# Kernel optimization log

Measured on AMD Instinct MI355X. Metric: run time of the kernel, lower is better.

Reference implementation:

```python
import jax, jax.numpy as jnp
import numpy as np

B = 256
N = 1024
K = 64
BASIS = 8
SINKHORN_ITERS = 1
TEMP = 0.2
EPS = 1e-5


def log_sinkhorn(log_alpha, n_iters=SINKHORN_ITERS, temperature=TEMP):
    la = log_alpha / temperature
    for _ in range(n_iters):
        la = la - jax.scipy.special.logsumexp(la, axis=-1, keepdims=True)
        la = la - jax.scipy.special.logsumexp(la, axis=-2, keepdims=True)
    return jnp.exp(la)


def setup_inputs() -> dict:
    key = jax.random.key(0)
    k1, k2, k3, k4 = jax.random.split(key, 4)
    x = jax.random.normal(k1, (B, N * K), dtype=jnp.float32)
    A_logits = 0.01 * jax.random.normal(k2, (N, N), dtype=jnp.float32)
    W_1 = 0.01 * jax.random.normal(k3, (N, BASIS), dtype=jnp.float32)
    W_V = 0.01 * jax.random.normal(k4, (BASIS, K, K), dtype=jnp.float32)
    gamma2 = jnp.ones((N,), dtype=jnp.float32)  # LayerNorm(N) weight
    beta2 = jnp.zeros((N,), dtype=jnp.float32)  # LayerNorm(N) bias
    return {"x": x, "A_logits": A_logits, "W_1": W_1, "W_V": W_V,
            "gamma2": gamma2, "beta2": beta2}


def layernorm(x, gamma, beta):
    mu = jnp.mean(x, axis=-1, keepdims=True)
    var = jnp.mean(jnp.square(x - mu), axis=-1, keepdims=True)
    return (x - mu) * jax.lax.rsqrt(var + EPS) * gamma + beta


def reference(x, A_logits, W_1, W_V, gamma2, beta2):
    x_reshaped = x.reshape(B, N, K)
    A = log_sinkhorn(A_logits)                       # [N, N] doubly-stochastic
    W_logits = jnp.einsum('tk,kde->tde', W_1, W_V)   # [N, K, K]
    W = log_sinkhorn(W_logits)                       # per-block doubly-stochastic
    x_local = jnp.einsum('bni,nio->bno', x_reshaped, W)  # N independent KxK GEMMs
    x_local = layernorm(jnp.transpose(x_local, (0, 2, 1)), gamma2, beta2)  # [B,K,N]
    x_global = x_local @ A                           # [B,K,N]
    x_global = jnp.transpose(x_global, (0, 2, 1))    # [B,N,K]
    return x_global.reshape(B, N * K)
```

## Files before the change

### kernel.cpp

```cpp
#include <hip/hip_runtime.h>
#include <hip/hip_fp16.h>
#include <math.h>

#define NDIM 1024
#define KDIM 64
#define BDIM 256
#define BKDIM 16384

typedef unsigned short u16;
typedef __attribute__((ext_vector_type(8))) short bf16x8;
typedef __attribute__((ext_vector_type(4))) float f32x4;

__device__ __forceinline__ float bf2f(u16 u) {
  union { unsigned u; float f; } x; x.u = ((unsigned)u) << 16; return x.f;
}
__device__ __forceinline__ u16 f2bf(float f) {
  union { float f; unsigned u; } x; x.f = f;
  unsigned u = x.u;
  u += 0x7fffu + ((u >> 16) & 1u);
  return (u16)(u >> 16);
}
__device__ __forceinline__ u16 f2h(float f) { return __half_as_ushort(__float2half(f)); }
__device__ __forceinline__ float h2f(u16 u) { return __half2float(__ushort_as_half(u)); }

__device__ __forceinline__ void async16(const u16* g, u16* s) {
  __builtin_amdgcn_global_load_lds(
      (const __attribute__((address_space(1))) unsigned int*)g,
      (__attribute__((address_space(3))) unsigned int*)s,
      16, 0, 0);
}

__global__ __launch_bounds__(256) void k_row_lse(const float* __restrict__ Alog,
                                                 float* __restrict__ r) {
  int m = blockIdx.x, t = threadIdx.x;
  float v[4], mx = -3.0e38f;
#pragma unroll
  for (int j = 0; j < 4; j++) {
    v[j] = Alog[m * NDIM + t + j * 256] * 5.0f;
    mx = fmaxf(mx, v[j]);
  }
  __shared__ float sred[256];
  sred[t] = mx; __syncthreads();
  for (int s = 128; s > 0; s >>= 1) { if (t < s) sred[t] = fmaxf(sred[t], sred[t + s]); __syncthreads(); }
  float bm = sred[0]; __syncthreads();
  float sm = 0.f;
#pragma unroll
  for (int j = 0; j < 4; j++) sm += __expf(v[j] - bm);
  sred[t] = sm; __syncthreads();
  for (int s = 128; s > 0; s >>= 1) { if (t < s) sred[t] += sred[t + s]; __syncthreads(); }
  if (t == 0) r[m] = bm + __logf(sred[0]);
}

__global__ __launch_bounds__(256) void k_col_dt(const float* __restrict__ Alog,
                                                const float* __restrict__ r,
                                                u16* __restrict__ Dt) {
  int n = blockIdx.x, t = threadIdx.x;
  float v[4], mx = -3.0e38f;
#pragma unroll
  for (int j = 0; j < 4; j++) {
    int m = t + j * 256;
    v[j] = Alog[m * NDIM + n] * 5.0f - r[m];
    mx = fmaxf(mx, v[j]);
  }
  __shared__ float sred[256];
  sred[t] = mx; __syncthreads();
  for (int s = 128; s > 0; s >>= 1) { if (t < s) sred[t] = fmaxf(sred[t], sred[t + s]); __syncthreads(); }
  float bm = sred[0]; __syncthreads();
  float sm = 0.f;
#pragma unroll
  for (int j = 0; j < 4; j++) sm += __expf(v[j] - bm);
  sred[t] = sm; __syncthreads();
  for (int s = 128; s > 0; s >>= 1) { if (t < s) sred[t] += sred[t + s]; __syncthreads(); }
  float cn = bm + __logf(sred[0]);
#pragma unroll
  for (int j = 0; j < 4; j++) {
    int m = t + j * 256;
    Dt[n * NDIM + m] = f2bf(__expf(v[j] - cn) - 0.0009765625f);
  }
}

__global__ __launch_bounds__(256) void k_w(const float* __restrict__ W1,
                                           const float* __restrict__ WV,
                                           u16* __restrict__ Wt) {
  int tb = blockIdx.x, t = threadIdx.x;
  int d = t >> 2, q = t & 3;
  float w1[8];
#pragma unroll
  for (int k = 0; k < 8; k++) w1[k] = W1[tb * 8 + k];
  float la[16];
#pragma unroll
  for (int j = 0; j < 16; j++) la[j] = 0.f;
#pragma unroll
  for (int k = 0; k < 8; k++) {
    float wk = w1[k];
    const float4* base = (const float4*)&WV[k * 4096 + d * 64 + q * 16];
#pragma unroll
    for (int v = 0; v < 4; v++) {
      float4 f = base[v];
      la[v * 4 + 0] += wk * f.x; la[v * 4 + 1] += wk * f.y;
      la[v * 4 + 2] += wk * f.z; la[v * 4 + 3] += wk * f.w;
    }
  }
  float mx = -3.0e38f;
#pragma unroll
  for (int j = 0; j < 16; j++) { la[j] *= 5.0f; mx = fmaxf(mx, la[j]); }
  float sm = 0.f;
#pragma unroll
  for (int j = 0; j < 16; j++) sm += __expf(la[j] - mx);
  for (int off = 1; off < 4; off <<= 1) {
    float mo = __shfl_xor(mx, off), so = __shfl_xor(sm, off);
    float mn = fmaxf(mx, mo);
    sm = sm * __expf(mx - mn) + so * __expf(mo - mn);
    mx = mn;
  }
  float rl = mx + __logf(sm);
  __shared__ float sla[64 * 65];
#pragma unroll
  for (int j = 0; j < 16; j++) sla[d * 65 + q * 16 + j] = la[j] - rl;
  __syncthreads();
  int e = t >> 2, jj = t & 3;
  float lb[16]; float m2 = -3.0e38f;
#pragma unroll
  for (int i = 0; i < 16; i++) { lb[i] = sla[(jj * 16 + i) * 65 + e]; m2 = fmaxf(m2, lb[i]); }
  float s2 = 0.f;
#pragma unroll
  for (int i = 0; i < 16; i++) s2 += __expf(lb[i] - m2);
  for (int off = 1; off < 4; off <<= 1) {
    float mo = __shfl_xor(m2, off), so = __shfl_xor(s2, off);
    float mn = fmaxf(m2, mo);
    s2 = s2 * __expf(m2 - mn) + so * __expf(mo - mn);
    m2 = mn;
  }
  float cl = m2 + __logf(s2);
#pragma unroll
  for (int i = 0; i < 16; i++)
    Wt[tb * 4096 + e * 64 + jj * 16 + i] = f2bf(__expf(lb[i] - cl));
}

__global__ __launch_bounds__(256) void k_gemm1(const float* __restrict__ x,
                                               const u16* __restrict__ Wt,
                                               u16* __restrict__ xl) {
  int n = blockIdx.x, t = threadIdx.x, w = t >> 6, l = t & 63;
  int q = l >> 4, lr = l & 15;
  const float* xb = x + n * 64;
  const u16* wb = Wt + n * 4096;
  f32x4 acc[4][4] = {};
#pragma unroll
  for (int ks = 0; ks < 2; ks++) {
    bf16x8 bfr[4];
#pragma unroll
    for (int ni = 0; ni < 4; ni++)
      bfr[ni] = *(const bf16x8*)&wb[(ni * 16 + lr) * 64 + ks * 32 + q * 8];
#pragma unroll
    for (int mi = 0; mi < 4; mi++) {
      int b = w * 64 + mi * 16 + lr;
      const float* xr = xb + (size_t)b * 65536 + ks * 32 + q * 8;
      float4 v0 = *(const float4*)xr;
      float4 v1 = *(const float4*)(xr + 4);
      float vf[8] = {v0.x, v0.y, v0.z, v0.w, v1.x, v1.y, v1.z, v1.w};
      bf16x8 ah, al;
#pragma unroll
      for (int j = 0; j < 8; j++) {
        u16 h = f2bf(vf[j]);
        ah[j] = (short)h;
        al[j] = (short)f2bf(vf[j] - bf2f(h));
      }
#pragma unroll
      for (int ni = 0; ni < 4; ni++) {
        acc[mi][ni] = __builtin_amdgcn_mfma_f32_16x16x32_bf16(ah, bfr[ni], acc[mi][ni], 0, 0, 0);
        acc[mi][ni] = __builtin_amdgcn_mfma_f32_16x16x32_bf16(al, bfr[ni], acc[mi][ni], 0, 0, 0);
      }
    }
  }
#pragma unroll
  for (int mi = 0; mi < 4; mi++)
#pragma unroll
    for (int ni = 0; ni < 4; ni++) {
      int o = ni * 16 + lr;
#pragma unroll
      for (int reg = 0; reg < 4; reg++) {
        int b = w * 64 + mi * 16 + q * 4 + reg;
        xl[n * BKDIM + b * 64 + o] = f2h(acc[mi][ni][reg]);
      }
    }
}

__global__ __launch_bounds__(256) void k_stat(const u16* __restrict__ xl,
                                              const float* __restrict__ g2,
                                              float* __restrict__ Ps,
                                              float* __restrict__ Pq,
                                              float* __restrict__ Pw) {
  __shared__ float sS[16 * 132], sQ[16 * 132], sW[16 * 132];
  int cb = blockIdx.x, mc = blockIdx.y, t = threadIdx.x;
  int c0 = cb * 128;
  int rg = t >> 4, cs = (t & 15) * 8;
  float sum[8], ssq[8], wg[8];
#pragma unroll
  for (int j = 0; j < 8; j++) { sum[j] = 0.f; ssq[j] = 0.f; wg[j] = 0.f; }
  for (int it = 0; it < 8; it++) {
    int row = mc * 128 + it * 16 + rg;
    bf16x8 v = *(const bf16x8*)&xl[(size_t)row * BKDIM + c0 + cs];
    float gm = g2[row];
#pragma unroll
    for (int j = 0; j < 8; j++) {
      float f = h2f((u16)v[j]);
      sum[j] += f; ssq[j] += f * f; wg[j] += f * gm;
    }
  }
#pragma unroll
  for (int j = 0; j < 8; j++) {
    sS[rg * 132 + cs + j] = sum[j];
    sQ[rg * 132 + cs + j] = ssq[j];
    sW[rg * 132 + cs + j] = wg[j];
  }
  __syncthreads();
  if (t < 128) {
    float S = 0.f, Q = 0.f, W = 0.f;
    for (int k = 0; k < 16; k++) {
      S += sS[k * 132 + t]; Q += sQ[k * 132 + t]; W += sW[k * 132 + t];
    }
    Ps[mc * BKDIM + c0 + t] = S;
    Pq[mc * BKDIM + c0 + t] = Q;
    Pw[mc * BKDIM + c0 + t] = W;
  }
}

__global__ __launch_bounds__(256) void k_fin(const float* __restrict__ Ps,
                                             const float* __restrict__ Pq,
                                             const float* __restrict__ Pw,
                                             const float* __restrict__ g2,
                                             const float* __restrict__ b2,
                                             float* __restrict__ mu,
                                             float* __restrict__ al,
                                             float* __restrict__ sON) {
  __shared__ float red[512];
  int t = threadIdx.x;
  float g = 0.f, b = 0.f;
#pragma unroll
  for (int k = 0; k < 4; k++) { g += g2[t * 4 + k]; b += b2[t * 4 + k]; }
  red[t] = g; red[256 + t] = b; __syncthreads();
  for (int s = 128; s > 0; s >>= 1) {
    if (t < s) { red[t] += red[t + s]; red[256 + t] += red[256 + t + s]; }
    __syncthreads();
  }
  float G = red[0], Bt = red[256];
  int bk = blockIdx.x * 256 + t;
  float S = 0.f, Q = 0.f, W = 0.f;
#pragma unroll
  for (int mc = 0; mc < 8; mc++) {
    S += Ps[mc * BKDIM + bk]; Q += Pq[mc * BKDIM + bk]; W += Pw[mc * BKDIM + bk];
  }
  float m_ = S * (1.0f / 1024.0f);
  float var = Q * (1.0f / 1024.0f) - m_ * m_;
  float a = rsqrtf(var + 1e-5f);
  mu[bk] = m_; al[bk] = a;
  sON[bk] = (a * (W - m_ * G) + Bt) * (1.0f / 1024.0f);
}

__global__ __launch_bounds__(256) void k_apply(const u16* __restrict__ xl,
                                               const float* __restrict__ g2,
                                               const float* __restrict__ b2,
                                               const float* __restrict__ mu,
                                               const float* __restrict__ al,
                                               u16* __restrict__ xln) {
  __shared__ __align__(16) u16 ldsT[128 * 128];
  int bkt = blockIdx.x, mc = blockIdx.y, t = threadIdx.x;
  int c0 = bkt * 128;
  int r = t >> 4, cs = t & 15;
  float mu8[8], al8[8];
#pragma unroll
  for (int j = 0; j < 8; j++) { mu8[j] = mu[c0 + cs * 8 + j]; al8[j] = al[c0 + cs * 8 + j]; }
  int key = cs << 3;
  for (int it = 0; it < 8; it++) {
    int m_ = it * 16 + r;
    int row = mc * 128 + m_;
    bf16x8 v = *(const bf16x8*)&xl[(size_t)row * BKDIM + c0 + cs * 8];
    float gm = g2[row], bt = b2[row];
    int pm = m_ ^ key;
#pragma unroll
    for (int j = 0; j < 8; j++) {
      float f = (h2f((u16)v[j]) - mu8[j]) * al8[j] * gm + bt;
      ldsT[(cs * 8 + j) * 128 + pm] = f2bf(f);
    }
  }
  __syncthreads();
  int ms = (t & 15) * 8;
  for (int it = 0; it < 8; it++) {
    int col = it * 16 + (t >> 4);
    int key2 = (col >> 3) << 3;
    bf16x8 o = *(const bf16x8*)&ldsT[col * 128 + (ms ^ key2)];
    *(bf16x8*)&xln[(size_t)(c0 + col) * NDIM + mc * 128 + ms] = o;
  }
}

__global__ __launch_bounds__(256) void k_gemm2(const u16* __restrict__ Dt,
                                               const u16* __restrict__ xln,
                                               const float* __restrict__ sON,
                                               float* __restrict__ out) {
  __shared__ __align__(16) u16 lA[128 * 64];
  __shared__ __align__(16) u16 lB[128 * 64];
  int bkt = blockIdx.x, n2t = blockIdx.y;
  int t = threadIdx.x, w = t >> 6, l = t & 63;
  int q = l >> 4, lr = l & 15;
  int rr = l >> 3;
  int cc = (l & 7) ^ rr;
  const u16* gA = Dt  + (size_t)(n2t * 128) * NDIM + cc * 8;
  const u16* gB = xln + (size_t)(bkt * 128) * NDIM + cc * 8;
  f32x4 acc[4][4] = {};
  for (int kt = 0; kt < 16; kt++) {
#pragma unroll
    for (int j = 0; j < 4; j++) {
      int ci = j * 4 + w;
      int row = ci * 8 + rr;
      async16(gA + (size_t)row * NDIM + kt * 64, &lA[ci * 512 + l * 8]);
      async16(gB + (size_t)row * NDIM + kt * 64, &lB[ci * 512 + l * 8]);
    }
    __syncthreads();
#pragma unroll
    for (int ks = 0; ks < 2; ks++) {
      int pc = ((ks * 4 + q) ^ (lr & 7)) * 8;
      bf16x8 af[4], bfr[4];
#pragma unroll
      for (int mi = 0; mi < 4; mi++)
        af[mi] = *(const bf16x8*)&lA[((w >> 1) * 64 + mi * 16 + lr) * 64 + pc];
#pragma unroll
      for (int ni = 0; ni < 4; ni++)
        bfr[ni] = *(const bf16x8*)&lB[((w & 1) * 64 + ni * 16 + lr) * 64 + pc];
#pragma unroll
      for (int mi = 0; mi < 4; mi++)
#pragma unroll
        for (int ni = 0; ni < 4; ni++)
          acc[mi][ni] = __builtin_amdgcn_mfma_f32_16x16x32_bf16(af[mi], bfr[ni], acc[mi][ni], 0, 0, 0);
    }
    __syncthreads();
  }
#pragma unroll
  for (int ni = 0; ni < 4; ni++) {
    int bk = bkt * 128 + (w & 1) * 64 + ni * 16 + lr;
    float sN = sON[bk];
    int b = bk >> 6, o = bk & 63;
#pragma unroll
    for (int mi = 0; mi < 4; mi++)
#pragma unroll
      for (int reg = 0; reg < 4; reg++) {
        int n2 = n2t * 128 + (w >> 1) * 64 + mi * 16 + q * 4 + reg;
        out[(size_t)b * 65536 + n2 * 64 + o] = acc[mi][ni][reg] + sN;
      }
  }
}

extern "C" void kernel_launch(void* const* d_in, const int* in_sizes, int n_in,
                              void* d_out, int out_size, void* d_ws, size_t ws_size,
                              hipStream_t stream) {
  const float* x    = (const float*)d_in[0];
  const float* Alog = (const float*)d_in[1];
  const float* W1   = (const float*)d_in[2];
  const float* WV   = (const float*)d_in[3];
  const float* g2   = (const float*)d_in[4];
  const float* b2   = (const float*)d_in[5];
  float* out = (float*)d_out;
  char* ws = (char*)d_ws;

  u16*   xln = (u16*)(ws);
  u16*   Wt  = (u16*)(ws + 33554432ull);
  u16*   Dt  = (u16*)(ws + 41943040ull);
  float* r   = (float*)(ws + 44040192ull);
  float* sON = (float*)(ws + 44044288ull);
  u16*   xl  = (u16*)((char*)d_out + 33554432ull);
  float* Ps  = (float*)((char*)d_out);
  float* Pq  = (float*)((char*)d_out + 524288ull);
  float* Pw  = (float*)((char*)d_out + 1048576ull);
  float* mu  = (float*)((char*)d_out + 1572864ull);
  float* al  = (float*)((char*)d_out + 1638400ull);

  k_row_lse<<<dim3(1024), dim3(256), 0, stream>>>(Alog, r);
  k_col_dt<<<dim3(1024), dim3(256), 0, stream>>>(Alog, r, Dt);
  k_w<<<dim3(1024), dim3(256), 0, stream>>>(W1, WV, Wt);
  k_gemm1<<<dim3(1024), dim3(256), 0, stream>>>(x, Wt, xl);
  k_stat<<<dim3(128, 8), dim3(256), 0, stream>>>(xl, g2, Ps, Pq, Pw);
  k_fin<<<dim3(64), dim3(256), 0, stream>>>(Ps, Pq, Pw, g2, b2, mu, al, sON);
  k_apply<<<dim3(128, 8), dim3(256), 0, stream>>>(xl, g2, b2, mu, al, xln);
  k_gemm2<<<dim3(128, 8), dim3(256), 0, stream>>>(Dt, xln, sON, out);
}
```

Measured before the change: 225.1 us.

## Fold LayerNorm affine into GEMM2 epilogue and A, drop separate apply pass

The LayerNorm scale gamma is folded into the transposed Sinkhorn matrix Dt, and the mean and beta terms become per-column corrections (gAc, bAc) plus per-row factors applied in the GEMM2 epilogue. This removes the k_apply pass that normalized and transposed the intermediate. GEMM1 now emits unnormalized bf16 in an interleaved N/8-blocked layout that GEMM2 can stream directly as its B operand, and each GEMM1 block processes 8 blocks of n for one 64-row batch tile. The intent is to cut one full read/write of the 32 MB intermediate and one launch. The trade-off is storing the unnormalized values in bf16 instead of fp16 and a heavier epilogue, which risks precision.

```diff
diff --git a/kernel.cpp b/kernel.cpp
--- a/kernel.cpp
+++ b/kernel.cpp
@@ -20,8 +20,6 @@
   u += 0x7fffu + ((u >> 16) & 1u);
   return (u16)(u >> 16);
 }
-__device__ __forceinline__ u16 f2h(float f) { return __half_as_ushort(__float2half(f)); }
-__device__ __forceinline__ float h2f(u16 u) { return __half2float(__ushort_as_half(u)); }
 
 __device__ __forceinline__ void async16(const u16* g, u16* s) {
   __builtin_amdgcn_global_load_lds(
@@ -51,9 +49,13 @@
   if (t == 0) r[m] = bm + __logf(sred[0]);
 }
 
-__global__ __launch_bounds__(256) void k_col_dt(const float* __restrict__ Alog,
-                                                const float* __restrict__ r,
-                                                u16* __restrict__ Dt) {
+__global__ __launch_bounds__(256) void k_col_dt2(const float* __restrict__ Alog,
+                                                 const float* __restrict__ r,
+                                                 const float* __restrict__ g2,
+                                                 const float* __restrict__ b2,
+                                                 u16* __restrict__ Dt,
+                                                 float* __restrict__ gAc,
+                                                 float* __restrict__ bAc) {
   int n = blockIdx.x, t = threadIdx.x;
   float v[4], mx = -3.0e38f;
 #pragma unroll
@@ -72,11 +74,23 @@
   sred[t] = sm; __syncthreads();
   for (int s = 128; s > 0; s >>= 1) { if (t < s) sred[t] += sred[t + s]; __syncthreads(); }
   float cn = bm + __logf(sred[0]);
+  float ga = 0.f, ba = 0.f;
 #pragma unroll
   for (int j = 0; j < 4; j++) {
     int m = t + j * 256;
-    Dt[n * NDIM + m] = f2bf(__expf(v[j] - cn) - 0.0009765625f);
-  }
+    float e = __expf(v[j] - cn);
+    float gm = g2[m];
+    Dt[n * NDIM + m] = f2bf(gm * (e - 0.0009765625f));
+    ga += gm * e; ba += b2[m] * e;
+  }
+  __syncthreads();
+  sred[t] = ga; __syncthreads();
+  for (int s = 128; s > 0; s >>= 1) { if (t < s) sred[t] += sred[t + s]; __syncthreads(); }
+  if (t == 0) gAc[n] = sred[0];
+  __syncthreads();
+  sred[t] = ba; __syncthreads();
+  for (int s = 128; s > 0; s >>= 1) { if (t < s) sred[t] += sred[t + s]; __syncthreads(); }
+  if (t == 0) bAc[n] = sred[0];
 }
 
 __global__ __launch_bounds__(256) void k_w(const float* __restrict__ W1,
@@ -137,24 +151,19 @@
     Wt[tb * 4096 + e * 64 + jj * 16 + i] = f2bf(__expf(lb[i] - cl));
 }
 
-__global__ __launch_bounds__(256) void k_gemm1(const float* __restrict__ x,
-                                               const u16* __restrict__ Wt,
-                                               u16* __restrict__ xl) {
-  int n = blockIdx.x, t = threadIdx.x, w = t >> 6, l = t & 63;
-  int q = l >> 4, lr = l & 15;
-  const float* xb = x + n * 64;
-  const u16* wb = Wt + n * 4096;
-  f32x4 acc[4][4] = {};
-#pragma unroll
-  for (int ks = 0; ks < 2; ks++) {
-    bf16x8 bfr[4];
-#pragma unroll
-    for (int ni = 0; ni < 4; ni++)
-      bfr[ni] = *(const bf16x8*)&wb[(ni * 16 + lr) * 64 + ks * 32 + q * 8];
-#pragma unroll
-    for (int mi = 0; mi < 4; mi++) {
-      int b = w * 64 + mi * 16 + lr;
-      const float* xr = xb + (size_t)b * 65536 + ks * 32 + q * 8;
+__global__ __launch_bounds__(256, 2) void k_gemm1b(const float* __restrict__ x,
+                                                   const u16* __restrict__ Wt,
+                                                   u16* __restrict__ xlb) {
+  int n8 = blockIdx.x, bt = blockIdx.y, t = threadIdx.x;
+  int w = t >> 6, l = t & 63, q = l >> 4, lr = l & 15;
+  int n0 = n8 * 8;
+  const float* xb = x + (size_t)(bt * 64 + w * 16 + lr) * 65536 + n0 * 64;
+  f32x4 acc[8][4] = {};
+#pragma unroll
+  for (int n = 0; n < 8; n++) {
+#pragma unroll
+    for (int ks = 0; ks < 2; ks++) {
+      const float* xr = xb + n * 64 + ks * 32 + q * 8;
       float4 v0 = *(const float4*)xr;
       float4 v1 = *(const float4*)(xr + 4);
       float vf[8] = {v0.x, v0.y, v0.z, v0.w, v1.x, v1.y, v1.z, v1.w};
@@ -167,136 +176,77 @@
       }
 #pragma unroll
       for (int ni = 0; ni < 4; ni++) {
-        acc[mi][ni] = __builtin_amdgcn_mfma_f32_16x16x32_bf16(ah, bfr[ni], acc[mi][ni], 0, 0, 0);
-        acc[mi][ni] = __builtin_amdgcn_mfma_f32_16x16x32_bf16(al, bfr[ni], acc[mi][ni], 0, 0, 0);
+        bf16x8 bfr = *(const bf16x8*)&Wt[(size_t)(n0 + n) * 4096 + (ni * 16 + lr) * 64 + ks * 32 + q * 8];
+        acc[n][ni] = __builtin_amdgcn_mfma_f32_16x16x32_bf16(ah, bfr, acc[n][ni], 0, 0, 0);
+        acc[n][ni] = __builtin_amdgcn_mfma_f32_16x16x32_bf16(al, bfr, acc[n][ni], 0, 0, 0);
       }
     }
   }
 #pragma unroll
-  for (int mi = 0; mi < 4; mi++)
-#pragma unroll
-    for (int ni = 0; ni < 4; ni++) {
-      int o = ni * 16 + lr;
-#pragma unroll
-      for (int reg = 0; reg < 4; reg++) {
-        int b = w * 64 + mi * 16 + q * 4 + reg;
-        xl[n * BKDIM + b * 64 + o] = f2h(acc[mi][ni][reg]);
-      }
-    }
-}
-
-__global__ __launch_bounds__(256) void k_stat(const u16* __restrict__ xl,
-                                              const float* __restrict__ g2,
-                                              float* __restrict__ Ps,
-                                              float* __restrict__ Pq,
-                                              float* __restrict__ Pw) {
-  __shared__ float sS[16 * 132], sQ[16 * 132], sW[16 * 132];
-  int cb = blockIdx.x, mc = blockIdx.y, t = threadIdx.x;
-  int c0 = cb * 128;
-  int rg = t >> 4, cs = (t & 15) * 8;
-  float sum[8], ssq[8], wg[8];
-#pragma unroll
-  for (int j = 0; j < 8; j++) { sum[j] = 0.f; ssq[j] = 0.f; wg[j] = 0.f; }
-  for (int it = 0; it < 8; it++) {
-    int row = mc * 128 + it * 16 + rg;
-    bf16x8 v = *(const bf16x8*)&xl[(size_t)row * BKDIM + c0 + cs];
-    float gm = g2[row];
+  for (int ni = 0; ni < 4; ni++) {
+#pragma unroll
+    for (int reg = 0; reg < 4; reg++) {
+      int bk = (bt * 64 + w * 16 + q * 4 + reg) * 64 + ni * 16 + lr;
+      bf16x8 o;
+#pragma unroll
+      for (int n = 0; n < 8; n++) o[n] = (short)f2bf(acc[n][ni][reg]);
+      *(bf16x8*)&xlb[((size_t)n8 * 16384 + bk) * 8] = o;
+    }
+  }
+}
+
+__global__ __launch_bounds__(256) void k_stat2(const u16* __restrict__ xlb,
+                                               const float* __restrict__ g2,
+                                               float* __restrict__ Ps,
+                                               float* __restrict__ Pq,
+                                               float* __restrict__ Pw) {
+  int t = threadIdx.x;
+  int bk = blockIdx.x * 256 + t;
+  int c = blockIdx.y;
+  float S = 0.f, Q = 0.f, W = 0.f;
+  for (int i = 0; i < 16; i++) {
+    int n8 = c * 16 + i;
+    bf16x8 v = *(const bf16x8*)&xlb[((size_t)n8 * 16384 + bk) * 8];
+    const float* gp = g2 + n8 * 8;
 #pragma unroll
     for (int j = 0; j < 8; j++) {
-      float f = h2f((u16)v[j]);
-      sum[j] += f; ssq[j] += f * f; wg[j] += f * gm;
-    }
-  }
-#pragma unroll
-  for (int j = 0; j < 8; j++) {
-    sS[rg * 132 + cs + j] = sum[j];
-    sQ[rg * 132 + cs + j] = ssq[j];
-    sW[rg * 132 + cs + j] = wg[j];
-  }
-  __syncthreads();
-  if (t < 128) {
-    float S = 0.f, Q = 0.f, W = 0.f;
-    for (int k = 0; k < 16; k++) {
-      S += sS[k * 132 + t]; Q += sQ[k * 132 + t]; W += sW[k * 132 + t];
-    }
-    Ps[mc * BKDIM + c0 + t] = S;
-    Pq[mc * BKDIM + c0 + t] = Q;
-    Pw[mc * BKDIM + c0 + t] = W;
-  }
-}
-
-__global__ __launch_bounds__(256) void k_fin(const float* __restrict__ Ps,
-                                             const float* __restrict__ Pq,
-                                             const float* __restrict__ Pw,
-                                             const float* __restrict__ g2,
-                                             const float* __restrict__ b2,
-                                             float* __restrict__ mu,
-                                             float* __restrict__ al,
-                                             float* __restrict__ sON) {
-  __shared__ float red[512];
-  int t = threadIdx.x;
-  float g = 0.f, b = 0.f;
-#pragma unroll
-  for (int k = 0; k < 4; k++) { g += g2[t * 4 + k]; b += b2[t * 4 + k]; }
-  red[t] = g; red[256 + t] = b; __syncthreads();
-  for (int s = 128; s > 0; s >>= 1) {
-    if (t < s) { red[t] += red[t + s]; red[256 + t] += red[256 + t + s]; }
-    __syncthreads();
-  }
-  float G = red[0], Bt = red[256];
-  int bk = blockIdx.x * 256 + t;
+      float f = bf2f((u16)v[j]);
+      S += f; Q += f * f; W += f * gp[j];
+    }
+  }
+  Ps[c * BKDIM + bk] = S;
+  Pq[c * BKDIM + bk] = Q;
+  Pw[c * BKDIM + bk] = W;
+}
+
+__global__ __launch_bounds__(256) void k_fin2(const float* __restrict__ Ps,
+                                              const float* __restrict__ Pq,
+                                              const float* __restrict__ Pw,
+                                              float* __restrict__ e1,
+                                              float* __restrict__ e2,
+                                              float* __restrict__ e3) {
+  int bk = blockIdx.x * 256 + threadIdx.x;
   float S = 0.f, Q = 0.f, W = 0.f;
 #pragma unroll
-  for (int mc = 0; mc < 8; mc++) {
-    S += Ps[mc * BKDIM + bk]; Q += Pq[mc * BKDIM + bk]; W += Pw[mc * BKDIM + bk];
+  for (int c = 0; c < 8; c++) {
+    S += Ps[c * BKDIM + bk]; Q += Pq[c * BKDIM + bk]; W += Pw[c * BKDIM + bk];
   }
   float m_ = S * (1.0f / 1024.0f);
   float var = Q * (1.0f / 1024.0f) - m_ * m_;
   float a = rsqrtf(var + 1e-5f);
-  mu[bk] = m_; al[bk] = a;
-  sON[bk] = (a * (W - m_ * G) + Bt) * (1.0f / 1024.0f);
-}
-
-__global__ __launch_bounds__(256) void k_apply(const u16* __restrict__ xl,
-                                               const float* __restrict__ g2,
-                                               const float* __restrict__ b2,
-                                               const float* __restrict__ mu,
-                                               const float* __restrict__ al,
-                                               u16* __restrict__ xln) {
-  __shared__ __align__(16) u16 ldsT[128 * 128];
-  int bkt = blockIdx.x, mc = blockIdx.y, t = threadIdx.x;
-  int c0 = bkt * 128;
-  int r = t >> 4, cs = t & 15;
-  float mu8[8], al8[8];
-#pragma unroll
-  for (int j = 0; j < 8; j++) { mu8[j] = mu[c0 + cs * 8 + j]; al8[j] = al[c0 + cs * 8 + j]; }
-  int key = cs << 3;
-  for (int it = 0; it < 8; it++) {
-    int m_ = it * 16 + r;
-    int row = mc * 128 + m_;
-    bf16x8 v = *(const bf16x8*)&xl[(size_t)row * BKDIM + c0 + cs * 8];
-    float gm = g2[row], bt = b2[row];
-    int pm = m_ ^ key;
-#pragma unroll
-    for (int j = 0; j < 8; j++) {
-      float f = (h2f((u16)v[j]) - mu8[j]) * al8[j] * gm + bt;
-      ldsT[(cs * 8 + j) * 128 + pm] = f2bf(f);
-    }
-  }
-  __syncthreads();
-  int ms = (t & 15) * 8;
-  for (int it = 0; it < 8; it++) {
-    int col = it * 16 + (t >> 4);
-    int key2 = (col >> 3) << 3;
-    bf16x8 o = *(const bf16x8*)&ldsT[col * 128 + (ms ^ key2)];
-    *(bf16x8*)&xln[(size_t)(c0 + col) * NDIM + mc * 128 + ms] = o;
-  }
-}
-
-__global__ __launch_bounds__(256) void k_gemm2(const u16* __restrict__ Dt,
-                                               const u16* __restrict__ xln,
-                                               const float* __restrict__ sON,
-                                               float* __restrict__ out) {
+  e1[bk] = a;
+  e2[bk] = a * W * (1.0f / 1024.0f);
+  e3[bk] = -a * m_;
+}
+
+__global__ __launch_bounds__(256) void k_gemm2b(const u16* __restrict__ Dt,
+                                                const u16* __restrict__ xlb,
+                                                const float* __restrict__ e1,
+                                                const float* __restrict__ e2,
+                                                const float* __restrict__ e3,
+                                                const float* __restrict__ gAc,
+                                                const float* __restrict__ bAc,
+                                                float* __restrict__ out) {
   __shared__ __align__(16) u16 lA[128 * 64];
   __shared__ __align__(16) u16 lB[128 * 64];
   int bkt = blockIdx.x, n2t = blockIdx.y;
@@ -304,16 +254,16 @@
   int q = l >> 4, lr = l & 15;
   int rr = l >> 3;
   int cc = (l & 7) ^ rr;
-  const u16* gA = Dt  + (size_t)(n2t * 128) * NDIM + cc * 8;
-  const u16* gB = xln + (size_t)(bkt * 128) * NDIM + cc * 8;
+  const u16* gAp = Dt + (size_t)(n2t * 128) * NDIM + cc * 8;
+  const u16* gBp = xlb + (size_t)cc * 131072 + (size_t)bkt * 1024 + rr * 8;
   f32x4 acc[4][4] = {};
   for (int kt = 0; kt < 16; kt++) {
 #pragma unroll
     for (int j = 0; j < 4; j++) {
       int ci = j * 4 + w;
       int row = ci * 8 + rr;
-      async16(gA + (size_t)row * NDIM + kt * 64, &lA[ci * 512 + l * 8]);
-      async16(gB + (size_t)row * NDIM + kt * 64, &lB[ci * 512 + l * 8]);
+      async16(gAp + (size_t)row * NDIM + kt * 64, &lA[ci * 512 + l * 8]);
+      async16(gBp + (size_t)kt * 1048576 + ci * 64, &lB[ci * 512 + l * 8]);
     }
     __syncthreads();
 #pragma unroll
@@ -337,14 +287,15 @@
 #pragma unroll
   for (int ni = 0; ni < 4; ni++) {
     int bk = bkt * 128 + (w & 1) * 64 + ni * 16 + lr;
-    float sN = sON[bk];
+    float a1 = e1[bk], a2 = e2[bk], a3 = e3[bk];
     int b = bk >> 6, o = bk & 63;
 #pragma unroll
     for (int mi = 0; mi < 4; mi++)
 #pragma unroll
       for (int reg = 0; reg < 4; reg++) {
         int n2 = n2t * 128 + (w >> 1) * 64 + mi * 16 + q * 4 + reg;
-        out[(size_t)b * 65536 + n2 * 64 + o] = acc[mi][ni][reg] + sN;
+        out[(size_t)b * 65536 + n2 * 64 + o] =
+            a1 * acc[mi][ni][reg] + a2 + a3 * gAc[n2] + bAc[n2];
       }
   }
 }
@@ -361,24 +312,24 @@
   float* out = (float*)d_out;
   char* ws = (char*)d_ws;
 
-  u16*   xln = (u16*)(ws);
+  u16*   xlb = (u16*)(ws);
   u16*   Wt  = (u16*)(ws + 33554432ull);
+  float* e1  = (float*)(ws + 33554432ull);
+  float* e2  = (float*)(ws + 33619968ull);
+  float* e3  = (float*)(ws + 33685504ull);
   u16*   Dt  = (u16*)(ws + 41943040ull);
   float* r   = (float*)(ws + 44040192ull);
-  float* sON = (float*)(ws + 44044288ull);
-  u16*   xl  = (u16*)((char*)d_out + 33554432ull);
+  float* gAc = (float*)(ws + 44044288ull);
+  float* bAc = (float*)(ws + 44048384ull);
   float* Ps  = (float*)((char*)d_out);
   float* Pq  = (float*)((char*)d_out + 524288ull);
   float* Pw  = (float*)((char*)d_out + 1048576ull);
-  float* mu  = (float*)((char*)d_out + 1572864ull);
-  float* al  = (float*)((char*)d_out + 1638400ull);
 
   k_row_lse<<<dim3(1024), dim3(256), 0, stream>>>(Alog, r);
-  k_col_dt<<<dim3(1024), dim3(256), 0, stream>>>(Alog, r, Dt);
+  k_col_dt2<<<dim3(1024), dim3(256), 0, stream>>>(Alog, r, g2, b2, Dt, gAc, bAc);
   k_w<<<dim3(1024), dim3(256), 0, stream>>>(W1, WV, Wt);
-  k_gemm1<<<dim3(1024), dim3(256), 0, stream>>>(x, Wt, xl);
-  k_stat<<<dim3(128, 8), dim3(256), 0, stream>>>(xl, g2, Ps, Pq, Pw);
-  k_fin<<<dim3(64), dim3(256), 0, stream>>>(Ps, Pq, Pw, g2, b2, mu, al, sON);
-  k_apply<<<dim3(128, 8), dim3(256), 0, stream>>>(xl, g2, b2, mu, al, xln);
-  k_gemm2<<<dim3(128, 8), dim3(256), 0, stream>>>(Dt, xln, sON, out);
-}
+  k_gemm1b<<<dim3(128, 4), dim3(256), 0, stream>>>(x, Wt, xlb);
+  k_stat2<<<dim3(64, 8), dim3(256), 0, stream>>>(xlb, g2, Ps, Pq, Pw);
+  k_fin2<<<dim3(64), dim3(256), 0, stream>>>(Ps, Pq, Pw, e1, e2, e3);
+  k_gemm2b<<<dim3(128, 8), dim3(256), 0, stream>>>(Dt, xlb, e1, e2, e3, gAc, bAc, out);
+}
```

Result: slower. 275.9 us (+22.6%).
